# Kernel tuning notes

Hardware: AMD Instinct MI355X
Metric: run time of the kernel (lower is better)

## Reference

```python
import jax, jax.numpy as jnp
import numpy as np

IN_FEATURES = 256
OUT_FEATURES = 256
GRID_SIZE = 5
SPLINE_ORDER = 3
GRID_RANGE = (-1.0, 1.0)
LN_EPS = 1e-5


def _make_grid():
    h = (GRID_RANGE[1] - GRID_RANGE[0]) / GRID_SIZE
    n_knots = GRID_SIZE + 2 * SPLINE_ORDER + 1  # 12
    return jnp.linspace(GRID_RANGE[0] - h * SPLINE_ORDER,
                        GRID_RANGE[1] + h * SPLINE_ORDER,
                        n_knots, dtype=jnp.float32)


def setup_inputs() -> dict:
    key = jax.random.key(0)
    k1, k2, k3 = jax.random.split(key, 3)
    N = 65536
    # kaiming_uniform_(nonlinearity='linear'): bound = sqrt(3/fan_in)
    b1 = np.sqrt(3.0 / IN_FEATURES)
    fan_sp = IN_FEATURES * (GRID_SIZE + SPLINE_ORDER)
    b2 = np.sqrt(3.0 / fan_sp)
    return {
        "x": jax.random.normal(k1, (N, IN_FEATURES), dtype=jnp.float32),
        "grid": _make_grid(),
        "base_weight": jax.random.uniform(k2, (OUT_FEATURES, IN_FEATURES), jnp.float32, -b1, b1),
        "spline_weight": jax.random.uniform(k3, (OUT_FEATURES, IN_FEATURES, GRID_SIZE + SPLINE_ORDER), jnp.float32, -b2, b2),
        "ln_gamma": jnp.ones((OUT_FEATURES,), jnp.float32),
        "ln_beta": jnp.zeros((OUT_FEATURES,), jnp.float32),
        "prelu_a": jnp.full((1,), 0.25, jnp.float32),
    }


def reference(x, grid, base_weight, spline_weight, ln_gamma, ln_beta, prelu_a):
    # base branch: exact GELU then linear (matches nn.GELU() + F.linear)
    base_out = jnp.einsum('ni,oi->no', jax.nn.gelu(x, approximate=False), base_weight)

    # Cox-de Boor B-spline basis recursion. grid is identical per feature in
    # the original ([in, 12] expand of a 1D linspace) so we broadcast the 1D grid.
    xu = x[:, :, None]                                   # [N, in, 1]
    bases = ((xu >= grid[:-1]) & (xu < grid[1:])).astype(x.dtype)  # [N, in, 11]
    for k in range(1, SPLINE_ORDER + 1):
        left = grid[:-(k + 1)]
        right = grid[k:-1]
        delta = jnp.where(right == left, jnp.ones_like(right), right - left)
        bases = ((xu - left) / delta * bases[:, :, :-1]
                 + (grid[k + 1:] - xu) / (grid[k + 1:] - grid[1:-k]) * bases[:, :, 1:])
    # bases: [N, in, grid_size + spline_order]

    spline_out = jnp.einsum('nig,oig->no', bases, spline_weight)

    y = base_out + spline_out
    mu = jnp.mean(y, axis=-1, keepdims=True)
    var = jnp.mean(jnp.square(y - mu), axis=-1, keepdims=True)
    y = (y - mu) * jax.lax.rsqrt(var + LN_EPS) * ln_gamma + ln_beta
    # PReLU with a single shared slope (nn.PReLU default)
    return jnp.where(y >= 0, y, prelu_a[0] * y)
```

## Files before the change

### kernel.cpp

```cpp
#include <hip/hip_runtime.h>
#include <hip/hip_bf16.h>
#include <math.h>
#include <stdint.h>

typedef __attribute__((ext_vector_type(8))) short short8;
typedef __attribute__((ext_vector_type(4))) float f32x4;

#define BM 256
#define NKT 36
#define A_BYTES (BM * 128)
#define LDS_TOTAL (2 * A_BYTES)

__device__ __forceinline__ unsigned short f2bf(float f) {
    union { float f; unsigned u; } c; c.f = f;
    unsigned u = c.u;
    unsigned r = u + 0x7fffu + ((u >> 16) & 1u);
    return (unsigned short)(r >> 16);
}

__device__ __forceinline__ float gelu_exact(float x) {
    return 0.5f * x * (1.0f + erff(x * 0.7071067811865475f));
}

__device__ __forceinline__ int swz(int row, int u) {
    return row * 128 + ((u ^ (row & 7)) << 4);
}

__global__ void kan_prep_w(const float* __restrict__ bw, const float* __restrict__ sw,
                           unsigned short* __restrict__ Wf) {
    int U = blockIdx.x * 256 + threadIdx.x;
    if (U >= NKT * 2048) return;
    int kt = U >> 11, rem = U & 2047;
    int wcq = rem >> 9, rem2 = rem & 511;
    int i = rem2 >> 6;
    int lane = rem2 & 63;
    int o = wcq * 64 + (i & 3) * 16 + (lane & 15);
    int k0 = kt * 64 + ((i >> 2) * 4 + (lane >> 4)) * 8;
    unsigned short pk[8];
#pragma unroll
    for (int e = 0; e < 8; ++e) {
        int kk = k0 + e;
        float v = (kk < 256) ? bw[o * 256 + kk] : sw[o * 2048 + (kk - 256)];
        pk[e] = f2bf(v);
    }
    *(short8*)(Wf + (size_t)U * 8) = *(short8*)pk;
}

__device__ __forceinline__ short8 spline_row(float xv) {
    float xi = (xv + 2.2f) * 2.5f;
    float fi = floorf(xi);
    float tt = xi - fi;
    float s1 = 1.0f - tt;
    float t2 = tt * tt, t3 = t2 * tt;
    float w0 = s1 * s1 * s1 * (1.0f / 6.0f);
    float w1 = 0.5f * t3 - t2 + (2.0f / 3.0f);
    float w2 = -0.5f * t3 + 0.5f * t2 + 0.5f * tt + (1.0f / 6.0f);
    float w3 = t3 * (1.0f / 6.0f);
    uint64_t Wp = (uint64_t)f2bf(w0) | ((uint64_t)f2bf(w1) << 16)
                | ((uint64_t)f2bf(w2) << 32) | ((uint64_t)f2bf(w3) << 48);
    int b = 16 * ((int)fi - 3);
    uint64_t L = (b >= 0 && b < 64) ? (Wp << b)
               : ((b < 0 && b > -64) ? (Wp >> (-b)) : 0ull);
    uint64_t H = (b >= 64 && b < 128) ? (Wp << (b - 64))
               : ((b > 0 && b < 64) ? (Wp >> (64 - b)) : 0ull);
    union { uint64_t q[2]; short8 v; } rr;
    rr.q[0] = L; rr.q[1] = H;
    return rr.v;
}

__global__ __launch_bounds__(512)
__attribute__((amdgpu_waves_per_eu(2, 2)))
void kan_fused(
    const float* __restrict__ X, const unsigned short* __restrict__ Wf,
    const float* __restrict__ gamma, const float* __restrict__ beta,
    const float* __restrict__ prelu_a, float* __restrict__ OUT)
{
    extern __shared__ __align__(16) unsigned char lds[];

    const int t = threadIdx.x;
    const int row0 = blockIdx.x * BM;
    const int wid = t >> 6, lane = t & 63;
    const int wr = wid >> 2, wc = wid & 3;
    const int lcol = lane & 15, q = lane >> 4;
    const int srow = t >> 3, scol = t & 7;

    f32x4 acc[8][4];
#pragma unroll
    for (int m = 0; m < 8; ++m)
#pragma unroll
        for (int n = 0; n < 4; ++n) acc[m][n] = (f32x4){0.f, 0.f, 0.f, 0.f};

    const unsigned short* wlane = Wf + ((size_t)wc * 512 + lane) * 8;

    short8 wv[8];
#pragma unroll
    for (int i = 0; i < 8; ++i)
        wv[i] = *(const short8*)(wlane + i * 512);
#pragma unroll
    for (int rep = 0; rep < 4; ++rep) {
        const float* xp = X + (size_t)(row0 + srow + rep * 64) * 256 + scol * 8;
        float4 v0 = *(const float4*)xp;
        float4 v1 = *(const float4*)(xp + 4);
        float vv[8] = {v0.x, v0.y, v0.z, v0.w, v1.x, v1.y, v1.z, v1.w};
        unsigned short pk[8];
#pragma unroll
        for (int j = 0; j < 8; ++j) pk[j] = f2bf(gelu_exact(vv[j]));
        *(short8*)(lds + swz(srow + rep * 64, scol)) = *(short8*)pk;
    }
    asm volatile("s_waitcnt lgkmcnt(0)\n\ts_barrier" ::: "memory");

    for (int kt = 0; kt < NKT; ++kt) {
        unsigned char* A_cur = lds + (kt & 1) * A_BYTES;
        unsigned char* A_nxt = lds + ((kt + 1) & 1) * A_BYTES;
        const bool has_next = (kt + 1 < NKT);
        const bool nxt_gelu = (kt + 1 < 4);

        float xs[4];
        if (has_next && !nxt_gelu) {
            const int ibase = (kt + 1 - 4) * 8;
#pragma unroll
            for (int rep = 0; rep < 4; ++rep)
                xs[rep] = X[(size_t)(row0 + srow + rep * 64) * 256 + ibase + scol];
        }

#pragma unroll
        for (int kh = 0; kh < 2; ++kh) {
            short8 af[8];
#pragma unroll
            for (int m = 0; m < 8; ++m)
                af[m] = *(const short8*)(A_cur + swz(wr * 128 + m * 16 + lcol, kh * 4 + q));
#pragma unroll
            for (int m = 0; m < 8; ++m)
#pragma unroll
                for (int n = 0; n < 4; ++n)
                    acc[m][n] = __builtin_amdgcn_mfma_f32_16x16x32_bf16(
                        af[m], wv[kh * 4 + n], acc[m][n], 0, 0, 0);
        }

        if (has_next) {
            const unsigned short* wsrc = wlane + (size_t)(kt + 1) * 2048 * 8;
#pragma unroll
            for (int i = 0; i < 8; ++i)
                wv[i] = *(const short8*)(wsrc + i * 512);

            if (nxt_gelu) {
#pragma unroll
                for (int rep = 0; rep < 4; ++rep) {
                    const float* xp = X + (size_t)(row0 + srow + rep * 64) * 256
                                    + (kt + 1) * 64 + scol * 8;
                    float4 v0 = *(const float4*)xp;
                    float4 v1 = *(const float4*)(xp + 4);
                    float vv[8] = {v0.x, v0.y, v0.z, v0.w, v1.x, v1.y, v1.z, v1.w};
                    unsigned short pk[8];
#pragma unroll
                    for (int j = 0; j < 8; ++j) pk[j] = f2bf(gelu_exact(vv[j]));
                    *(short8*)(A_nxt + swz(srow + rep * 64, scol)) = *(short8*)pk;
                }
            } else {
#pragma unroll
                for (int rep = 0; rep < 4; ++rep)
                    *(short8*)(A_nxt + swz(srow + rep * 64, scol)) = spline_row(xs[rep]);
            }
        }
        asm volatile("s_waitcnt lgkmcnt(0)\n\ts_barrier" ::: "memory");
    }

    float* stats = (float*)lds;
#pragma unroll
    for (int m = 0; m < 8; ++m) {
#pragma unroll
        for (int r = 0; r < 4; ++r) {
            float s = 0.f, s2 = 0.f;
#pragma unroll
            for (int n = 0; n < 4; ++n) { float v = acc[m][n][r]; s += v; s2 += v * v; }
#pragma unroll
            for (int msk = 1; msk < 16; msk <<= 1) {
                s  += __shfl_xor(s,  msk, 64);
                s2 += __shfl_xor(s2, msk, 64);
            }
            if ((lane & 15) == ((m * 4 + r) & 15)) {
                int row = wr * 128 + m * 16 + q * 4 + r;
                stats[row * 8 + wc]     = s;
                stats[row * 8 + 4 + wc] = s2;
            }
        }
    }
    __syncthreads();

    const float apr = prelu_a[0];
    float gv[4], bv[4];
#pragma unroll
    for (int n = 0; n < 4; ++n) {
        int col = wc * 64 + n * 16 + lcol;
        gv[n] = gamma[col]; bv[n] = beta[col];
    }
#pragma unroll
    for (int m = 0; m < 8; ++m) {
#pragma unroll
        for (int r = 0; r < 4; ++r) {
            int row = wr * 128 + m * 16 + q * 4 + r;
            f32x4 sv = *(const f32x4*)(stats + row * 8);
            f32x4 qv = *(const f32x4*)(stats + row * 8 + 4);
            float mu  = (sv[0] + sv[1] + sv[2] + sv[3]) * (1.0f / 256.0f);
            float ex2 = (qv[0] + qv[1] + qv[2] + qv[3]) * (1.0f / 256.0f);
            float rs = rsqrtf(ex2 - mu * mu + 1e-5f);
            float* op = OUT + (size_t)(row0 + row) * 256;
#pragma unroll
            for (int n = 0; n < 4; ++n) {
                int col = wc * 64 + n * 16 + lcol;
                float y = (acc[m][n][r] - mu) * rs * gv[n] + bv[n];
                op[col] = (y >= 0.f) ? y : apr * y;
            }
        }
    }
}

extern "C" void kernel_launch(void* const* d_in, const int* in_sizes, int n_in,
                              void* d_out, int out_size, void* d_ws, size_t ws_size,
                              hipStream_t stream) {
    const float* x  = (const float*)d_in[0];
    const float* bw = (const float*)d_in[2];
    const float* sw = (const float*)d_in[3];
    const float* g  = (const float*)d_in[4];
    const float* be = (const float*)d_in[5];
    const float* pa = (const float*)d_in[6];
    float* out = (float*)d_out;
    unsigned short* Wf = (unsigned short*)d_ws;

    hipFuncSetAttribute((const void*)kan_fused,
                        hipFuncAttributeMaxDynamicSharedMemorySize, LDS_TOTAL);

    const int Nrows = in_sizes[0] / 256;
    kan_prep_w<<<(NKT * 2048 + 255) / 256, 256, 0, stream>>>(bw, sw, Wf);
    kan_fused<<<Nrows / BM, 512, LDS_TOTAL, stream>>>(x, Wf, g, be, pa, out);
}
```

Baseline: 127.1 us.

## Use four LDS stages, processing two K-tiles per barrier

```diff
diff --git a/kernel.cpp b/kernel.cpp
--- a/kernel.cpp
+++ b/kernel.cpp
@@ -9,13 +9,11 @@
 #define BM 256
 #define NKT 36
 #define A_BYTES (BM * 128)
-#define LDS_TOTAL (2 * A_BYTES)
+#define LDS_TOTAL (4 * A_BYTES)
 
 __device__ __forceinline__ unsigned short f2bf(float f) {
-    union { float f; unsigned u; } c; c.f = f;
-    unsigned u = c.u;
-    unsigned r = u + 0x7fffu + ((u >> 16) & 1u);
-    return (unsigned short)(r >> 16);
+    __bf16 h = (__bf16)f;
+    return __builtin_bit_cast(unsigned short, h);
 }
 
 __device__ __forceinline__ float gelu_exact(float x) {
@@ -69,7 +67,6 @@
 }
 
 __global__ __launch_bounds__(512)
-__attribute__((amdgpu_waves_per_eu(2, 2)))
 void kan_fused(
     const float* __restrict__ X, const unsigned short* __restrict__ Wf,
     const float* __restrict__ gamma, const float* __restrict__ beta,
@@ -91,44 +88,39 @@
         for (int n = 0; n < 4; ++n) acc[m][n] = (f32x4){0.f, 0.f, 0.f, 0.f};
 
     const unsigned short* wlane = Wf + ((size_t)wc * 512 + lane) * 8;
-
     short8 wv[8];
-#pragma unroll
-    for (int i = 0; i < 8; ++i)
-        wv[i] = *(const short8*)(wlane + i * 512);
-#pragma unroll
-    for (int rep = 0; rep < 4; ++rep) {
-        const float* xp = X + (size_t)(row0 + srow + rep * 64) * 256 + scol * 8;
-        float4 v0 = *(const float4*)xp;
-        float4 v1 = *(const float4*)(xp + 4);
-        float vv[8] = {v0.x, v0.y, v0.z, v0.w, v1.x, v1.y, v1.z, v1.w};
-        unsigned short pk[8];
-#pragma unroll
-        for (int j = 0; j < 8; ++j) pk[j] = f2bf(gelu_exact(vv[j]));
-        *(short8*)(lds + swz(srow + rep * 64, scol)) = *(short8*)pk;
-    }
-    asm volatile("s_waitcnt lgkmcnt(0)\n\ts_barrier" ::: "memory");
-
-    for (int kt = 0; kt < NKT; ++kt) {
-        unsigned char* A_cur = lds + (kt & 1) * A_BYTES;
-        unsigned char* A_nxt = lds + ((kt + 1) & 1) * A_BYTES;
-        const bool has_next = (kt + 1 < NKT);
-        const bool nxt_gelu = (kt + 1 < 4);
-
-        float xs[4];
-        if (has_next && !nxt_gelu) {
-            const int ibase = (kt + 1 - 4) * 8;
-#pragma unroll
-            for (int rep = 0; rep < 4; ++rep)
-                xs[rep] = X[(size_t)(row0 + srow + rep * 64) * 256 + ibase + scol];
-        }
-
+
+    auto w_load = [&](int kt) {
+        const unsigned short* wsrc = wlane + (size_t)kt * 2048 * 8;
+#pragma unroll
+        for (int i = 0; i < 8; ++i)
+            wv[i] = *(const short8*)(wsrc + i * 512);
+    };
+    auto gelu_stage = [&](int kt, unsigned char* D) {
+#pragma unroll
+        for (int rep = 0; rep < 4; ++rep) {
+            const float* xp = X + (size_t)(row0 + srow + rep * 64) * 256 + kt * 64 + scol * 8;
+            float4 v0 = *(const float4*)xp;
+            float4 v1 = *(const float4*)(xp + 4);
+            float vv[8] = {v0.x, v0.y, v0.z, v0.w, v1.x, v1.y, v1.z, v1.w};
+            unsigned short pk[8];
+#pragma unroll
+            for (int jj = 0; jj < 8; ++jj) pk[jj] = f2bf(gelu_exact(vv[jj]));
+            *(short8*)(D + swz(srow + rep * 64, scol)) = *(short8*)pk;
+        }
+    };
+    auto spline_stage = [&](float (&xs)[4], unsigned char* D) {
+#pragma unroll
+        for (int rep = 0; rep < 4; ++rep)
+            *(short8*)(D + swz(srow + rep * 64, scol)) = spline_row(xs[rep]);
+    };
+    auto mfma_tile = [&](unsigned char* B) {
 #pragma unroll
         for (int kh = 0; kh < 2; ++kh) {
             short8 af[8];
 #pragma unroll
             for (int m = 0; m < 8; ++m)
-                af[m] = *(const short8*)(A_cur + swz(wr * 128 + m * 16 + lcol, kh * 4 + q));
+                af[m] = *(const short8*)(B + swz(wr * 128 + m * 16 + lcol, kh * 4 + q));
 #pragma unroll
             for (int m = 0; m < 8; ++m)
 #pragma unroll
@@ -136,32 +128,43 @@
                     acc[m][n] = __builtin_amdgcn_mfma_f32_16x16x32_bf16(
                         af[m], wv[kh * 4 + n], acc[m][n], 0, 0, 0);
         }
-
-        if (has_next) {
-            const unsigned short* wsrc = wlane + (size_t)(kt + 1) * 2048 * 8;
-#pragma unroll
-            for (int i = 0; i < 8; ++i)
-                wv[i] = *(const short8*)(wsrc + i * 512);
-
-            if (nxt_gelu) {
-#pragma unroll
-                for (int rep = 0; rep < 4; ++rep) {
-                    const float* xp = X + (size_t)(row0 + srow + rep * 64) * 256
-                                    + (kt + 1) * 64 + scol * 8;
-                    float4 v0 = *(const float4*)xp;
-                    float4 v1 = *(const float4*)(xp + 4);
-                    float vv[8] = {v0.x, v0.y, v0.z, v0.w, v1.x, v1.y, v1.z, v1.w};
-                    unsigned short pk[8];
-#pragma unroll
-                    for (int j = 0; j < 8; ++j) pk[j] = f2bf(gelu_exact(vv[j]));
-                    *(short8*)(A_nxt + swz(srow + rep * 64, scol)) = *(short8*)pk;
-                }
-            } else {
-#pragma unroll
-                for (int rep = 0; rep < 4; ++rep)
-                    *(short8*)(A_nxt + swz(srow + rep * 64, scol)) = spline_row(xs[rep]);
-            }
-        }
+    };
+
+    w_load(0);
+    gelu_stage(0, lds);
+    gelu_stage(1, lds + A_BYTES);
+    asm volatile("s_waitcnt lgkmcnt(0)\n\ts_barrier" ::: "memory");
+
+    for (int j = 0; j < NKT / 2; ++j) {
+        const int ka = 2 * j, kb = ka + 1;
+        unsigned char* Ba = lds + (ka & 3) * A_BYTES;
+        unsigned char* Bb = lds + (kb & 3) * A_BYTES;
+        unsigned char* Sa = lds + ((ka + 2) & 3) * A_BYTES;
+        unsigned char* Sb = lds + ((ka + 3) & 3) * A_BYTES;
+        const bool stg = (ka + 2 < NKT);
+        const bool gA = (ka + 2 < 4), gB = (ka + 3 < 4);
+
+        float xsA[4], xsB[4];
+        if (stg && !gA) {
+            const int ibA = (ka + 2 - 4) * 8;
+#pragma unroll
+            for (int rep = 0; rep < 4; ++rep)
+                xsA[rep] = X[(size_t)(row0 + srow + rep * 64) * 256 + ibA + scol];
+        }
+        if (stg && !gB) {
+            const int ibB = (ka + 3 - 4) * 8;
+#pragma unroll
+            for (int rep = 0; rep < 4; ++rep)
+                xsB[rep] = X[(size_t)(row0 + srow + rep * 64) * 256 + ibB + scol];
+        }
+
+        mfma_tile(Ba);
+        w_load(kb);
+        if (stg) { if (gA) gelu_stage(ka + 2, Sa); else spline_stage(xsA, Sa); }
+        mfma_tile(Bb);
+        if (ka + 2 < NKT) w_load(ka + 2);
+        if (stg) { if (gB) gelu_stage(ka + 3, Sb); else spline_stage(xsB, Sb); }
+
         asm volatile("s_waitcnt lgkmcnt(0)\n\ts_barrier" ::: "memory");
     }
 
```

Measured after the change: 126.5 us. No clear change (-0.4%).

## Compute spline basis in registers from transposed bf16 x tile in LDS

Applied to the files above, without the earlier changes.

```diff
diff --git a/kernel.cpp b/kernel.cpp
--- a/kernel.cpp
+++ b/kernel.cpp
@@ -8,14 +8,13 @@
 
 #define BM 256
 #define NKT 36
-#define A_BYTES (BM * 128)
-#define LDS_TOTAL (2 * A_BYTES)
+#define XT_BYTES (256 * 512)
+#define G_BYTES (BM * 128)
+#define LDS_TOTAL (XT_BYTES + G_BYTES)
 
 __device__ __forceinline__ unsigned short f2bf(float f) {
-    union { float f; unsigned u; } c; c.f = f;
-    unsigned u = c.u;
-    unsigned r = u + 0x7fffu + ((u >> 16) & 1u);
-    return (unsigned short)(r >> 16);
+    __bf16 h = (__bf16)f;
+    return __builtin_bit_cast(unsigned short, h);
 }
 
 __device__ __forceinline__ float gelu_exact(float x) {
@@ -76,6 +75,7 @@
     const float* __restrict__ prelu_a, float* __restrict__ OUT)
 {
     extern __shared__ __align__(16) unsigned char lds[];
+    unsigned char* G = lds + XT_BYTES;
 
     const int t = threadIdx.x;
     const int row0 = blockIdx.x * BM;
@@ -91,80 +91,89 @@
         for (int n = 0; n < 4; ++n) acc[m][n] = (f32x4){0.f, 0.f, 0.f, 0.f};
 
     const unsigned short* wlane = Wf + ((size_t)wc * 512 + lane) * 8;
-
     short8 wv[8];
-#pragma unroll
-    for (int i = 0; i < 8; ++i)
-        wv[i] = *(const short8*)(wlane + i * 512);
-#pragma unroll
-    for (int rep = 0; rep < 4; ++rep) {
-        const float* xp = X + (size_t)(row0 + srow + rep * 64) * 256 + scol * 8;
-        float4 v0 = *(const float4*)xp;
-        float4 v1 = *(const float4*)(xp + 4);
-        float vv[8] = {v0.x, v0.y, v0.z, v0.w, v1.x, v1.y, v1.z, v1.w};
-        unsigned short pk[8];
-#pragma unroll
-        for (int j = 0; j < 8; ++j) pk[j] = f2bf(gelu_exact(vv[j]));
-        *(short8*)(lds + swz(srow + rep * 64, scol)) = *(short8*)pk;
-    }
-    asm volatile("s_waitcnt lgkmcnt(0)\n\ts_barrier" ::: "memory");
-
-    for (int kt = 0; kt < NKT; ++kt) {
-        unsigned char* A_cur = lds + (kt & 1) * A_BYTES;
-        unsigned char* A_nxt = lds + ((kt + 1) & 1) * A_BYTES;
-        const bool has_next = (kt + 1 < NKT);
-        const bool nxt_gelu = (kt + 1 < 4);
-
-        float xs[4];
-        if (has_next && !nxt_gelu) {
-            const int ibase = (kt + 1 - 4) * 8;
-#pragma unroll
-            for (int rep = 0; rep < 4; ++rep)
-                xs[rep] = X[(size_t)(row0 + srow + rep * 64) * 256 + ibase + scol];
-        }
-
+    auto w_load = [&](int kt) {
+        const unsigned short* wsrc = wlane + (size_t)kt * 2048 * 8;
+#pragma unroll
+        for (int i = 0; i < 8; ++i)
+            wv[i] = *(const short8*)(wsrc + i * 512);
+    };
+    auto mfma_tile_lds = [&](unsigned char* B) {
 #pragma unroll
         for (int kh = 0; kh < 2; ++kh) {
-            short8 af[8];
-#pragma unroll
-            for (int m = 0; m < 8; ++m)
-                af[m] = *(const short8*)(A_cur + swz(wr * 128 + m * 16 + lcol, kh * 4 + q));
-#pragma unroll
-            for (int m = 0; m < 8; ++m)
+#pragma unroll
+            for (int m = 0; m < 8; ++m) {
+                short8 af = *(const short8*)(B + swz(wr * 128 + m * 16 + lcol, kh * 4 + q));
 #pragma unroll
                 for (int n = 0; n < 4; ++n)
                     acc[m][n] = __builtin_amdgcn_mfma_f32_16x16x32_bf16(
-                        af[m], wv[kh * 4 + n], acc[m][n], 0, 0, 0);
-        }
-
-        if (has_next) {
-            const unsigned short* wsrc = wlane + (size_t)(kt + 1) * 2048 * 8;
-#pragma unroll
-            for (int i = 0; i < 8; ++i)
-                wv[i] = *(const short8*)(wsrc + i * 512);
-
-            if (nxt_gelu) {
-#pragma unroll
-                for (int rep = 0; rep < 4; ++rep) {
-                    const float* xp = X + (size_t)(row0 + srow + rep * 64) * 256
-                                    + (kt + 1) * 64 + scol * 8;
-                    float4 v0 = *(const float4*)xp;
-                    float4 v1 = *(const float4*)(xp + 4);
-                    float vv[8] = {v0.x, v0.y, v0.z, v0.w, v1.x, v1.y, v1.z, v1.w};
-                    unsigned short pk[8];
-#pragma unroll
-                    for (int j = 0; j < 8; ++j) pk[j] = f2bf(gelu_exact(vv[j]));
-                    *(short8*)(A_nxt + swz(srow + rep * 64, scol)) = *(short8*)pk;
-                }
-            } else {
-#pragma unroll
-                for (int rep = 0; rep < 4; ++rep)
-                    *(short8*)(A_nxt + swz(srow + rep * 64, scol)) = spline_row(xs[rep]);
-            }
-        }
-        asm volatile("s_waitcnt lgkmcnt(0)\n\ts_barrier" ::: "memory");
-    }
-
+                        af, wv[kh * 4 + n], acc[m][n], 0, 0, 0);
+            }
+        }
+    };
+
+#pragma unroll
+    for (int rb = 0; rb < 4; ++rb) {
+#pragma unroll
+        for (int cb = 0; cb < 4; ++cb) {
+            int row = rb * 64 + srow;
+            int c0 = cb * 64 + scol * 8;
+            const float* xp = X + (size_t)(row0 + row) * 256 + c0;
+            float4 v0 = *(const float4*)xp;
+            float4 v1 = *(const float4*)(xp + 4);
+            float vv[8] = {v0.x, v0.y, v0.z, v0.w, v1.x, v1.y, v1.z, v1.w};
+#pragma unroll
+            for (int jj = 0; jj < 8; ++jj)
+                *(unsigned short*)(lds + (c0 + jj) * 512 + row * 2) = f2bf(vv[jj]);
+        }
+    }
+
+#pragma unroll
+    for (int kt = 0; kt < 4; ++kt) {
+        w_load(kt);
+#pragma unroll
+        for (int rep = 0; rep < 4; ++rep) {
+            const float* xp = X + (size_t)(row0 + srow + rep * 64) * 256 + kt * 64 + scol * 8;
+            float4 v0 = *(const float4*)xp;
+            float4 v1 = *(const float4*)(xp + 4);
+            float vv[8] = {v0.x, v0.y, v0.z, v0.w, v1.x, v1.y, v1.z, v1.w};
+            unsigned short pk[8];
+#pragma unroll
+            for (int jj = 0; jj < 8; ++jj) pk[jj] = f2bf(gelu_exact(vv[jj]));
+            *(short8*)(G + swz(srow + rep * 64, scol)) = *(short8*)pk;
+        }
+        __syncthreads();
+        mfma_tile_lds(G);
+        __syncthreads();
+    }
+
+    const unsigned char* xbase = lds + q * 512 + wr * 256 + lcol * 2;
+    for (int kt = 4; kt < NKT; ++kt) {
+        w_load(kt);
+        const unsigned char* xb = xbase + (kt - 4) * 4096;
+        float xf[16];
+#pragma unroll
+        for (int kh = 0; kh < 2; ++kh)
+#pragma unroll
+            for (int m = 0; m < 8; ++m) {
+                unsigned short xv = *(const unsigned short*)(xb + kh * 2048 + m * 32);
+                union { unsigned u; float f; } cc; cc.u = ((unsigned)xv) << 16;
+                xf[kh * 8 + m] = cc.f;
+            }
+#pragma unroll
+        for (int kh = 0; kh < 2; ++kh) {
+#pragma unroll
+            for (int m = 0; m < 8; ++m) {
+                short8 af = spline_row(xf[kh * 8 + m]);
+#pragma unroll
+                for (int n = 0; n < 4; ++n)
+                    acc[m][n] = __builtin_amdgcn_mfma_f32_16x16x32_bf16(
+                        af, wv[kh * 4 + n], acc[m][n], 0, 0, 0);
+            }
+        }
+    }
+
+    __syncthreads();
     float* stats = (float*)lds;
 #pragma unroll
     for (int m = 0; m < 8; ++m) {
```

Result: slower. 176.8 us (+39.2%).
